# Performance work log

Hardware: AMD Instinct MI355X
Metric: run time of the kernel (lower is better)

## Reference

```python
import jax, jax.numpy as jnp
import numpy as np

THRESHOLD = 0.15  # init kwarg


def setup_inputs() -> dict:
    key = jax.random.key(0)
    B, T, N = 64, 1024, 512
    inputs = jax.random.normal(key, (B, T, N), dtype=jnp.float32)
    return {"inputs": inputs}


def reference(inputs) -> jnp.ndarray:
    # inputs: [B, T, N]; Pearson correlation across the sample (time) axis.
    B, T, N = inputs.shape
    xc = inputs - jnp.mean(inputs, axis=1, keepdims=True)        # [B,T,N]
    cov = jnp.einsum('bti,btj->bij', xc, xc)                     # [B,N,N] (unnormalized; norm cancels)
    d = jnp.sqrt(jnp.diagonal(cov, axis1=1, axis2=2))            # [B,N]
    corr = cov / (d[:, :, None] * d[:, None, :])                 # [B,N,N]

    # Original loop: for i<j, if |corr[:,i,j]|>thr: mask = mask * one_hot(i).
    # Equivalent closed form: let fired[b,i] = any_{j>i} |corr[b,i,j]|>thr.
    #   0 fired rows -> all-ones mask
    #   1 fired row  -> one_hot of that i (repeated onehot(i) multiplies are idempotent)
    #   >=2 distinct fired rows -> onehot(i1)*onehot(i2)=0 -> all-zeros mask
    upper = jnp.triu(jnp.ones((N, N), dtype=bool), k=1)
    cond = (jnp.abs(corr) > THRESHOLD) & upper                   # [B,N,N]
    fired = jnp.any(cond, axis=2)                                # [B,N]
    num_fired = jnp.sum(fired, axis=1)                           # [B]

    ones = jnp.ones((B, N), dtype=jnp.float32)
    mask = jnp.where((num_fired == 0)[:, None], ones,
                     jnp.where((num_fired == 1)[:, None],
                               fired.astype(jnp.float32),
                               jnp.zeros_like(ones)))
    return mask
```

## Files before the change

kernel.cpp:

```cpp
#include <hip/hip_runtime.h>
#include <hip/hip_bf16.h>

#define BB 64
#define TT 1024
#define NN 512
#define LISTCAP (1u << 18)

static constexpr float THR = 0.15f;

typedef __attribute__((ext_vector_type(8))) short bf16x8;
typedef __attribute__((ext_vector_type(4))) float f32x4;

__device__ __forceinline__ void gload16(const void* g, void* lds_dst) {
    __builtin_amdgcn_global_load_lds(
        (const __attribute__((address_space(1))) unsigned int*)g,
        (__attribute__((address_space(3))) unsigned int*)lds_dst, 16, 0, 0);
}

__global__ __launch_bounds__(512) void transpose_colsum(
    const float* __restrict__ x, ushort* __restrict__ xbf,
    float* __restrict__ s1, float* __restrict__ dv,
    float* __restrict__ nv, float* __restrict__ nl,
    unsigned* __restrict__ fired, unsigned* __restrict__ cnt) {
    __shared__ ushort tile[64 * 512];
    __shared__ float red[3][8][64];
    int b = blockIdx.x, ng = blockIdx.y;
    int n0 = ng * 64;
    int tid = threadIdx.x, w = tid >> 6, l = tid & 63;
    const float* xb = x + (size_t)b * TT * NN;
    float a1 = 0.f, a2 = 0.f, al = 0.f;
    unsigned swz = ((unsigned)l & 7u) << 4;

    if (b == 0 && ng == 0 && tid == 64) *cnt = 0;

    for (int tc = 0; tc < 2; ++tc) {
        for (int i = 0; i < 8; ++i) {
            int tl0 = i * 64 + w * 8;
            int t0 = tc * 512 + tl0;
            unsigned hp[4];
            #pragma unroll
            for (int q = 0; q < 4; ++q) {
                float v0 = xb[(size_t)(t0 + 2 * q) * NN + n0 + l];
                float v1 = xb[(size_t)(t0 + 2 * q + 1) * NN + n0 + l];
                a1 += v0 + v1;
                a2 += v0 * v0 + v1 * v1;
                unsigned u0 = __float_as_uint(v0), u1 = __float_as_uint(v1);
                float h0 = __uint_as_float(u0 & 0xFFFF0000u);
                float h1 = __uint_as_float(u1 & 0xFFFF0000u);
                float l0 = v0 - h0, l1 = v1 - h1;
                al += l0 * l0 + l1 * l1;
                hp[q] = (u0 >> 16) | (u1 & 0xFFFF0000u);
            }
            unsigned off = (unsigned)l * 1024u + (((unsigned)tl0 * 2u) ^ swz);
            *(uint4*)((char*)tile + off) = make_uint4(hp[0], hp[1], hp[2], hp[3]);
        }
        __syncthreads();
        #pragma unroll
        for (int cc = 0; cc < 8; ++cc) {
            int cl = w * 8 + cc;
            unsigned src = (unsigned)cl * 1024u
                           + (((unsigned)l * 16u) ^ (((unsigned)cl & 7u) << 4));
            uint4 val = *(const uint4*)((char*)tile + src);
            ushort* dst = xbf + ((size_t)(b * NN + n0 + cl) * TT + tc * 512 + l * 8);
            *(uint4*)dst = val;
        }
        __syncthreads();
    }
    red[0][w][l] = a1; red[1][w][l] = a2; red[2][w][l] = al;
    __syncthreads();
    if (tid < 64) {
        float r1 = 0.f, r2 = 0.f, rl = 0.f;
        #pragma unroll
        for (int k = 0; k < 8; ++k) {
            r1 += red[0][k][tid]; r2 += red[1][k][tid]; rl += red[2][k][tid];
        }
        size_t o = (size_t)b * NN + n0 + tid;
        s1[o] = r1;
        dv[o] = r2 - r1 * r1 * (1.0f / TT);
        nv[o] = sqrtf(r2);
        nl[o] = sqrtf(rl);
        fired[o] = 0u;
    }
}

__global__ __launch_bounds__(64) void corr_mfma(
    const ushort* __restrict__ xbf, const float* __restrict__ s1,
    const float* __restrict__ dv, const float* __restrict__ nv,
    const float* __restrict__ nl, unsigned* __restrict__ fired,
    unsigned* __restrict__ cnt, unsigned* __restrict__ list) {
    __shared__ uint4 ldsbuf[1024];
    char* base = (char*)ldsbuf;

    int id = blockIdx.x;
    int swz = ((id & 7) * 288) + (id >> 3);
    int b = swz / 36;
    int u = swz % 36;
    int ti = 0, rem = u;
    while (rem >= (8 - ti)) { rem -= (8 - ti); ++ti; }
    int tj = ti + rem;
    int i0 = ti * 64, j0 = tj * 64;
    bool diag = (ti == tj);

    int lane = threadIdx.x & 63;
    int rl = lane & 15, kg = lane >> 4;

    int cq = lane >> 2;
    int kk = (lane & 3) ^ ((lane >> 3) & 3);
    const ushort* xb = xbf + (size_t)b * NN * TT;
    const ushort* srcA = xb + (size_t)(i0 + cq) * TT + kk * 8;
    const ushort* srcB = xb + (size_t)(j0 + cq) * TT + kk * 8;

    auto STAGE = [&](int t0, int buf) {
        char* dbase = base + (buf << 13);
        #pragma unroll
        for (int q = 0; q < 4; ++q)
            gload16(srcA + (size_t)q * 16 * TT + t0, dbase + q * 1024);
        if (!diag) {
            #pragma unroll
            for (int q = 0; q < 4; ++q)
                gload16(srcB + (size_t)q * 16 * TT + t0, dbase + 4096 + q * 1024);
        }
    };

    unsigned aoff[4], boff[4];
    #pragma unroll
    for (int f = 0; f < 4; ++f) {
        unsigned ca = (unsigned)(16 * f + rl);
        unsigned o = ca * 64u + ((((unsigned)kg ^ ((ca >> 1) & 3u)) & 3u) << 4);
        aoff[f] = o;
        boff[f] = o;
    }
    unsigned bbase = diag ? 0u : 4096u;

    f32x4 acc[4][4];
    #pragma unroll
    for (int i = 0; i < 4; ++i)
        #pragma unroll
        for (int j = 0; j < 4; ++j)
            acc[i][j] = (f32x4)0.0f;

    STAGE(0, 0);
    for (int it = 0; it < 32; ++it) {
        asm volatile("s_waitcnt vmcnt(0)" ::: "memory");
        __builtin_amdgcn_sched_barrier(0);
        if (it + 1 < 32) STAGE((it + 1) * 32, (it + 1) & 1);
        __builtin_amdgcn_sched_barrier(0);
        const char* cb = base + ((it & 1) << 13);
        bf16x8 A[4], Bv[4];
        #pragma unroll
        for (int f = 0; f < 4; ++f) A[f] = *(const bf16x8*)(cb + aoff[f]);
        #pragma unroll
        for (int f = 0; f < 4; ++f) Bv[f] = *(const bf16x8*)(cb + bbase + boff[f]);
        #pragma unroll
        for (int fj = 0; fj < 4; ++fj)
            #pragma unroll
            for (int fi = 0; fi < 4; ++fi)
                acc[fi][fj] = __builtin_amdgcn_mfma_f32_16x16x32_bf16(
                    A[fi], Bv[fj], acc[fi][fj], 0, 0, 0);
    }

    const float thr2 = THR * THR;
    const float invT = 1.0f / TT;
    const float* s1b = s1 + (size_t)b * NN;
    const float* dvb = dv + (size_t)b * NN;
    const float* nvb = nv + (size_t)b * NN;
    const float* nlb = nl + (size_t)b * NN;
    unsigned* fb = fired + (size_t)b * NN;
    int rowb = i0 + kg * 4;
    int colb = j0 + rl;
    #pragma unroll
    for (int fj = 0; fj < 4; ++fj) {
        int gj = colb + 16 * fj;
        float sj = s1b[gj], djv = dvb[gj];
        float nvj = nvb[gj], nlj = nlb[gj];
        #pragma unroll
        for (int fi = 0; fi < 4; ++fi) {
            int gi0 = rowb + 16 * fi;
            #pragma unroll
            for (int r = 0; r < 4; ++r) {
                int gi = gi0 + r;
                if (gj > gi) {
                    float cc = acc[fi][fj][r] - s1b[gi] * sj * invT;
                    float lim = thr2 * dvb[gi] * djv;
                    float nvi = nvb[gi], nli = nlb[gi];
                    float B = nli * nvj + nlj * nvi + 3.0f * nli * nlj
                              + 1e-3f * nvi * nvj;
                    float a = fabsf(cc);
                    float lo = a - B;
                    if (lo > 0.0f && lo * lo > lim) {
                        atomicOr(&fb[gi], 1u);
                    } else if ((a + B) * (a + B) > lim) {
                        unsigned idx = atomicAdd(cnt, 1u);
                        if (idx < LISTCAP)
                            list[idx] = ((unsigned)b << 18) | ((unsigned)gi << 9)
                                        | (unsigned)gj;
                    }
                }
            }
        }
    }
}

__global__ __launch_bounds__(256) void cleanup_pairs(
    const float* __restrict__ x, const float* __restrict__ s1,
    const float* __restrict__ dv, const unsigned* __restrict__ cnt,
    const unsigned* __restrict__ list, unsigned* __restrict__ fired) {
    unsigned n = *cnt;
    if (n > LISTCAP) n = LISTCAP;
    int lane = threadIdx.x & 63;
    int gw = (blockIdx.x * 256 + threadIdx.x) >> 6;
    int nw = (gridDim.x * 256) >> 6;
    for (unsigned p = gw; p < n; p += nw) {
        unsigned e = list[p];
        int b = e >> 18, i = (e >> 9) & 511, j = e & 511;
        const float* xb = x + (size_t)b * TT * NN;
        double s = 0.0;
        for (int t = lane; t < TT; t += 64)
            s += (double)xb[(size_t)t * NN + i] * (double)xb[(size_t)t * NN + j];
        #pragma unroll
        for (int o = 32; o > 0; o >>= 1)
            s += __shfl_xor(s, o, 64);
        if (lane == 0) {
            double cov = s - (double)s1[(size_t)b * NN + i]
                             * (double)s1[(size_t)b * NN + j] / (double)TT;
            double lim = (double)THR * (double)THR
                         * (double)dv[(size_t)b * NN + i]
                         * (double)dv[(size_t)b * NN + j];
            if (cov * cov > lim) atomicOr(&fired[(size_t)b * NN + i], 1u);
        }
    }
}

__global__ __launch_bounds__(512) void finalize_mask(
    const unsigned* __restrict__ fired, float* __restrict__ out) {
    int b = blockIdx.x;
    int n = threadIdx.x;
    unsigned f = fired[(size_t)b * NN + n];
    __shared__ int wsum[8];
    unsigned long long m = __ballot(f != 0u);
    int lane = n & 63;
    int w = n >> 6;
    if (lane == 0) wsum[w] = __popcll(m);
    __syncthreads();
    int cnt = 0;
    #pragma unroll
    for (int i = 0; i < 8; ++i) cnt += wsum[i];
    float val = (cnt == 0) ? 1.0f : ((cnt == 1) ? (f ? 1.0f : 0.0f) : 0.0f);
    out[(size_t)b * NN + n] = val;
}

extern "C" void kernel_launch(void* const* d_in, const int* in_sizes, int n_in,
                              void* d_out, int out_size, void* d_ws, size_t ws_size,
                              hipStream_t stream) {
    const float* x = (const float*)d_in[0];
    float* out = (float*)d_out;

    ushort* xbf = (ushort*)d_ws;
    float* s1 = (float*)(xbf + (size_t)BB * NN * TT);
    float* dv = s1 + (size_t)BB * NN;
    float* nv = dv + (size_t)BB * NN;
    float* nl = nv + (size_t)BB * NN;
    unsigned* fired = (unsigned*)(nl + (size_t)BB * NN);
    unsigned* cnt   = fired + (size_t)BB * NN;
    unsigned* list  = cnt + 16;

    transpose_colsum<<<dim3(BB, 8), 512, 0, stream>>>(x, xbf, s1, dv, nv, nl,
                                                      fired, cnt);
    corr_mfma<<<dim3(2304), 64, 0, stream>>>(xbf, s1, dv, nv, nl, fired, cnt, list);
    cleanup_pairs<<<128, 256, 0, stream>>>(x, s1, dv, cnt, list, fired);
    finalize_mask<<<BB, 512, 0, stream>>>(fired, out);
}
```

Before: 97.45 us.

## Pre-tile bf16 operand layout and split correlation tiles across four waves

The transpose kernel now writes bf16 data straight into a pre-swizzled, tile-contiguous layout (64 columns × 32 time steps per 4 KB chunk). This drops the LDS transpose and its two barriers. The MFMA kernel uses 256 threads per block: each of four waves computes a 32×32 quadrant, one contiguous 16-byte global-to-LDS load per thread stages each chunk, and waves skip the redundant lower quadrant on diagonal tiles. In exchange it adds a block barrier every iteration, and the staging loads no longer wait on vmcnt explicitly before the next buffer is read, so correctness depends on the barrier covering those loads.

```diff
diff --git a/kernel.cpp b/kernel.cpp
--- a/kernel.cpp
+++ b/kernel.cpp
@@ -22,26 +22,27 @@
     float* __restrict__ s1, float* __restrict__ dv,
     float* __restrict__ nv, float* __restrict__ nl,
     unsigned* __restrict__ fired, unsigned* __restrict__ cnt) {
-    __shared__ ushort tile[64 * 512];
     __shared__ float red[3][8][64];
     int b = blockIdx.x, ng = blockIdx.y;
     int n0 = ng * 64;
     int tid = threadIdx.x, w = tid >> 6, l = tid & 63;
-    const float* xb = x + (size_t)b * TT * NN;
+    const float* xb = x + (size_t)b * TT * NN + n0 + l;
     float a1 = 0.f, a2 = 0.f, al = 0.f;
-    unsigned swz = ((unsigned)l & 7u) << 4;
-
     if (b == 0 && ng == 0 && tid == 64) *cnt = 0;
 
+    char* xbase = (char*)xbf + ((size_t)(b * 8 + ng) * 32) * 4096
+                  + (unsigned)l * 64u
+                  + (((unsigned)(w & 3) ^ (((unsigned)l >> 1) & 3u)) << 4);
+
     for (int tc = 0; tc < 2; ++tc) {
+        #pragma unroll
         for (int i = 0; i < 8; ++i) {
-            int tl0 = i * 64 + w * 8;
-            int t0 = tc * 512 + tl0;
+            int t0 = tc * 512 + i * 64 + w * 8;
             unsigned hp[4];
             #pragma unroll
             for (int q = 0; q < 4; ++q) {
-                float v0 = xb[(size_t)(t0 + 2 * q) * NN + n0 + l];
-                float v1 = xb[(size_t)(t0 + 2 * q + 1) * NN + n0 + l];
+                float v0 = xb[(size_t)(t0 + 2 * q) * NN];
+                float v1 = xb[(size_t)(t0 + 2 * q + 1) * NN];
                 a1 += v0 + v1;
                 a2 += v0 * v0 + v1 * v1;
                 unsigned u0 = __float_as_uint(v0), u1 = __float_as_uint(v1);
@@ -51,20 +52,9 @@
                 al += l0 * l0 + l1 * l1;
                 hp[q] = (u0 >> 16) | (u1 & 0xFFFF0000u);
             }
-            unsigned off = (unsigned)l * 1024u + (((unsigned)tl0 * 2u) ^ swz);
-            *(uint4*)((char*)tile + off) = make_uint4(hp[0], hp[1], hp[2], hp[3]);
-        }
-        __syncthreads();
-        #pragma unroll
-        for (int cc = 0; cc < 8; ++cc) {
-            int cl = w * 8 + cc;
-            unsigned src = (unsigned)cl * 1024u
-                           + (((unsigned)l * 16u) ^ (((unsigned)cl & 7u) << 4));
-            uint4 val = *(const uint4*)((char*)tile + src);
-            ushort* dst = xbf + ((size_t)(b * NN + n0 + cl) * TT + tc * 512 + l * 8);
-            *(uint4*)dst = val;
-        }
-        __syncthreads();
+            *(uint4*)(xbase + (size_t)(t0 >> 5) * 4096) =
+                make_uint4(hp[0], hp[1], hp[2], hp[3]);
+        }
     }
     red[0][w][l] = a1; red[1][w][l] = a2; red[2][w][l] = al;
     __syncthreads();
@@ -83,7 +73,7 @@
     }
 }
 
-__global__ __launch_bounds__(64) void corr_mfma(
+__global__ __launch_bounds__(256, 8) void corr_mfma(
     const ushort* __restrict__ xbf, const float* __restrict__ s1,
     const float* __restrict__ dv, const float* __restrict__ nv,
     const float* __restrict__ nl, unsigned* __restrict__ fired,
@@ -101,62 +91,60 @@
     int i0 = ti * 64, j0 = tj * 64;
     bool diag = (ti == tj);
 
-    int lane = threadIdx.x & 63;
+    int tid = threadIdx.x;
+    int wave = tid >> 6, lane = tid & 63;
     int rl = lane & 15, kg = lane >> 4;
 
-    int cq = lane >> 2;
-    int kk = (lane & 3) ^ ((lane >> 3) & 3);
-    const ushort* xb = xbf + (size_t)b * NN * TT;
-    const ushort* srcA = xb + (size_t)(i0 + cq) * TT + kk * 8;
-    const ushort* srcB = xb + (size_t)(j0 + cq) * TT + kk * 8;
-
-    auto STAGE = [&](int t0, int buf) {
-        char* dbase = base + (buf << 13);
-        #pragma unroll
-        for (int q = 0; q < 4; ++q)
-            gload16(srcA + (size_t)q * 16 * TT + t0, dbase + q * 1024);
-        if (!diag) {
-            #pragma unroll
-            for (int q = 0; q < 4; ++q)
-                gload16(srcB + (size_t)q * 16 * TT + t0, dbase + 4096 + q * 1024);
-        }
+    const char* srcA = (const char*)xbf + ((size_t)(b * 8 + ti) * 32) * 4096 + tid * 16;
+    const char* srcB = (const char*)xbf + ((size_t)(b * 8 + tj) * 32) * 4096 + tid * 16;
+
+    auto STAGE = [&](int s, int buf) {
+        char* d = base + (buf << 13) + wave * 1024;
+        gload16(srcA + (size_t)s * 4096, d);
+        if (!diag) gload16(srcB + (size_t)s * 4096, d + 4096);
     };
 
-    unsigned aoff[4], boff[4];
-    #pragma unroll
-    for (int f = 0; f < 4; ++f) {
-        unsigned ca = (unsigned)(16 * f + rl);
-        unsigned o = ca * 64u + ((((unsigned)kg ^ ((ca >> 1) & 3u)) & 3u) << 4);
-        aoff[f] = o;
-        boff[f] = o;
+    int wr = wave >> 1, wc = wave & 1;
+    bool skip_mm = diag && (wr == 1) && (wc == 0);
+
+    unsigned aoff[2], boff[2];
+    #pragma unroll
+    for (int f = 0; f < 2; ++f) {
+        unsigned ca = (unsigned)(32 * wr + 16 * f + rl);
+        aoff[f] = ca * 64u + ((((unsigned)kg ^ ((ca >> 1) & 3u)) & 3u) << 4);
+        unsigned cb2 = (unsigned)(32 * wc + 16 * f + rl);
+        boff[f] = cb2 * 64u + ((((unsigned)kg ^ ((cb2 >> 1) & 3u)) & 3u) << 4);
     }
     unsigned bbase = diag ? 0u : 4096u;
 
-    f32x4 acc[4][4];
-    #pragma unroll
-    for (int i = 0; i < 4; ++i)
-        #pragma unroll
-        for (int j = 0; j < 4; ++j)
+    f32x4 acc[2][2];
+    #pragma unroll
+    for (int i = 0; i < 2; ++i)
+        #pragma unroll
+        for (int j = 0; j < 2; ++j)
             acc[i][j] = (f32x4)0.0f;
 
     STAGE(0, 0);
+    __syncthreads();
+
     for (int it = 0; it < 32; ++it) {
-        asm volatile("s_waitcnt vmcnt(0)" ::: "memory");
-        __builtin_amdgcn_sched_barrier(0);
-        if (it + 1 < 32) STAGE((it + 1) * 32, (it + 1) & 1);
-        __builtin_amdgcn_sched_barrier(0);
+        if (it + 1 < 32) STAGE(it + 1, (it + 1) & 1);
+
         const char* cb = base + ((it & 1) << 13);
-        bf16x8 A[4], Bv[4];
-        #pragma unroll
-        for (int f = 0; f < 4; ++f) A[f] = *(const bf16x8*)(cb + aoff[f]);
-        #pragma unroll
-        for (int f = 0; f < 4; ++f) Bv[f] = *(const bf16x8*)(cb + bbase + boff[f]);
-        #pragma unroll
-        for (int fj = 0; fj < 4; ++fj)
-            #pragma unroll
-            for (int fi = 0; fi < 4; ++fi)
-                acc[fi][fj] = __builtin_amdgcn_mfma_f32_16x16x32_bf16(
-                    A[fi], Bv[fj], acc[fi][fj], 0, 0, 0);
+        if (!skip_mm) {
+            bf16x8 A[2], Bv[2];
+            #pragma unroll
+            for (int f = 0; f < 2; ++f) A[f] = *(const bf16x8*)(cb + aoff[f]);
+            #pragma unroll
+            for (int f = 0; f < 2; ++f) Bv[f] = *(const bf16x8*)(cb + bbase + boff[f]);
+            #pragma unroll
+            for (int fj = 0; fj < 2; ++fj)
+                #pragma unroll
+                for (int fi = 0; fi < 2; ++fi)
+                    acc[fi][fj] = __builtin_amdgcn_mfma_f32_16x16x32_bf16(
+                        A[fi], Bv[fj], acc[fi][fj], 0, 0, 0);
+        }
+        __syncthreads();
     }
 
     const float thr2 = THR * THR;
@@ -166,15 +154,15 @@
     const float* nvb = nv + (size_t)b * NN;
     const float* nlb = nl + (size_t)b * NN;
     unsigned* fb = fired + (size_t)b * NN;
-    int rowb = i0 + kg * 4;
-    int colb = j0 + rl;
-    #pragma unroll
-    for (int fj = 0; fj < 4; ++fj) {
+    int rowb = i0 + 32 * wr + kg * 4;
+    int colb = j0 + 32 * wc + rl;
+    #pragma unroll
+    for (int fj = 0; fj < 2; ++fj) {
         int gj = colb + 16 * fj;
         float sj = s1b[gj], djv = dvb[gj];
         float nvj = nvb[gj], nlj = nlb[gj];
         #pragma unroll
-        for (int fi = 0; fi < 4; ++fi) {
+        for (int fi = 0; fi < 2; ++fi) {
             int gi0 = rowb + 16 * fi;
             #pragma unroll
             for (int r = 0; r < 4; ++r) {
@@ -266,7 +254,7 @@
 
     transpose_colsum<<<dim3(BB, 8), 512, 0, stream>>>(x, xbf, s1, dv, nv, nl,
                                                       fired, cnt);
-    corr_mfma<<<dim3(2304), 64, 0, stream>>>(xbf, s1, dv, nv, nl, fired, cnt, list);
+    corr_mfma<<<dim3(2304), 256, 0, stream>>>(xbf, s1, dv, nv, nl, fired, cnt, list);
     cleanup_pairs<<<128, 256, 0, stream>>>(x, s1, dv, cnt, list, fired);
     finalize_mask<<<BB, 512, 0, stream>>>(fired, out);
 }
```

Result: faster. 87.36 us (-10.4%).
